# Optimization experiments

Hardware: AMD Instinct MI355X
Metric: run time of the kernel (lower is better)

The kernel has to match this reference:

```python
import jax, jax.numpy as jnp
import numpy as np

N = 50000     # num_nodes
E = 600000    # num_edges
H = 128       # h_dim
OUT = 32      # out_dim
R = 64        # num_rels
B = 16        # num_bases


def setup_inputs() -> dict:
    key = jax.random.key(0)
    ks = jax.random.split(key, 11)
    src = jax.random.randint(ks[0], (E,), 0, N)
    dst = jax.random.randint(ks[1], (E,), 0, N)
    etype = jax.random.randint(ks[2], (E,), 0, R)
    norm = jax.random.uniform(ks[3], (E, 1), dtype=jnp.float32)  # edge norm (e.g. 1/deg)
    emb = jax.random.normal(ks[4], (N, H), dtype=jnp.float32) * 0.05
    # basis-decomposed relation weights: W_r = sum_b comp[r,b] * V[b]
    V1 = jax.random.normal(ks[5], (B, H, H), dtype=jnp.float32) * (1.0 / np.sqrt(H))
    comp1 = jax.random.normal(ks[6], (R, B), dtype=jnp.float32) * (1.0 / np.sqrt(B))
    bias1 = jnp.zeros((H,), dtype=jnp.float32)
    V2 = jax.random.normal(ks[7], (B, H, OUT), dtype=jnp.float32) * (1.0 / np.sqrt(H))
    comp2 = jax.random.normal(ks[8], (R, B), dtype=jnp.float32) * (1.0 / np.sqrt(B))
    bias2 = jnp.zeros((OUT,), dtype=jnp.float32)
    return {"src": src, "dst": dst, "etype": etype, "norm": norm, "emb": emb,
            "V1": V1, "comp1": comp1, "bias1": bias1,
            "V2": V2, "comp2": comp2, "bias2": bias2}


def _rel_graph_conv(x, src, dst, etype, norm, V, comp, bias):
    # message for edge e: (x[src_e] @ W_{etype_e}) * norm_e, W_r = sum_b comp[r,b] V_b.
    # Since W is linear, fold norm into the gathered features, and aggregate
    # per (dst, basis) BEFORE the dense basis matmul (aggregate-first trick):
    #   agg[v, b] = sum_{e: dst_e=v} comp[etype_e, b] * norm_e * x[src_e]
    #   out[v]    = sum_b agg[v, b] @ V_b + bias
    xs = x[src] * norm                      # [E, in]
    w = comp[etype]                         # [E, B] per-edge basis coefficients
    # loop over the small fixed basis count (B=16), reusing the [E, in] buffer
    agg = jnp.stack(
        [jax.ops.segment_sum(xs * w[:, b:b + 1], dst, num_segments=N) for b in range(B)],
        axis=1,
    )                                       # [N, B, in]
    return jnp.einsum('nbi,bio->no', agg, V) + bias


def reference(src, dst, etype, norm, emb, V1, comp1, bias1, V2, comp2, bias2):
    h = _rel_graph_conv(emb, src, dst, etype, norm, V1, comp1, bias1)
    h = jax.nn.relu(h)                      # dropout p=0.0 -> identity
    h = _rel_graph_conv(h, src, dst, etype, norm, V2, comp2, bias2)
    return h
```

## Files before the change

kernel.cpp:

```cpp
#include <hip/hip_runtime.h>
#include <hip/hip_bf16.h>

#define NN 50000
#define EE 600000
#define HH 128
#define OUTD 32
#define RR 64
#define BB 16
#define KK 2048
#define SC_B ((NN + 1023) / 1024)
#define N_CONVW ((HH + OUTD) * KK)
#define N_EMB   (NN * HH / 2)

typedef short s16x8 __attribute__((ext_vector_type(8)));
typedef float f32x4 __attribute__((ext_vector_type(4)));
typedef float f32x2 __attribute__((ext_vector_type(2)));
typedef unsigned short ushort_t;
typedef unsigned int uint_t;
typedef __attribute__((address_space(3))) uint_t lds_u32;
typedef const __attribute__((address_space(1))) uint_t glb_u32;

__device__ inline ushort_t f_to_bf16(float f){
    __hip_bfloat16 h = __float2bfloat16(f);
    return *reinterpret_cast<ushort_t*>(&h);
}
__device__ inline uint_t pack_bf16x2(float a, float b){
    return (uint_t)f_to_bf16(a) | ((uint_t)f_to_bf16(b) << 16);
}

__global__ void hist_kernel(const int* __restrict__ dst, int* counts){
    int e = blockIdx.x*256 + threadIdx.x;
    if (e < EE) atomicAdd(&counts[dst[e]], 1);
}

__global__ void scan_part(const int* __restrict__ counts, int* __restrict__ tot){
    int b = blockIdx.x, t = threadIdx.x;
    int i0 = b*1024 + t*4;
    int s = 0;
    if (i0 + 3 < NN){
        int4 v = *reinterpret_cast<const int4*>(&counts[i0]);
        s = v.x + v.y + v.z + v.w;
    } else {
        for (int j = 0; j < 4; j++) if (i0 + j < NN) s += counts[i0 + j];
    }
    #pragma unroll
    for (int off = 32; off; off >>= 1) s += __shfl_xor(s, off, 64);
    __shared__ int ws[4];
    if ((t & 63) == 0) ws[t >> 6] = s;
    __syncthreads();
    if (t == 0) tot[b] = ws[0] + ws[1] + ws[2] + ws[3];
}

__global__ void scan_tot(int* tot){
    int t = threadIdx.x;
    int v = (t < SC_B) ? tot[t] : 0;
    int x = v;
    #pragma unroll
    for (int off = 1; off < 64; off <<= 1){
        int y = __shfl_up(x, off, 64);
        if (t >= off) x += y;
    }
    if (t < SC_B) tot[t] = x - v;
}

__global__ void scan_final(const int* __restrict__ counts, const int* __restrict__ tot,
                           int* __restrict__ offsets, int* __restrict__ cursor){
    int b = blockIdx.x, t = threadIdx.x, lane = t & 63, wv = t >> 6;
    int i0 = b*1024 + t*4;
    int v[4]; int s = 0;
    #pragma unroll
    for (int j = 0; j < 4; j++){ v[j] = (i0 + j < NN) ? counts[i0 + j] : 0; s += v[j]; }
    int x = s;
    #pragma unroll
    for (int off = 1; off < 64; off <<= 1){
        int y = __shfl_up(x, off, 64);
        if (lane >= off) x += y;
    }
    __shared__ int ws[4];
    if (lane == 63) ws[wv] = x;
    __syncthreads();
    int pre = tot[b];
    for (int i = 0; i < wv; i++) pre += ws[i];
    int run = pre + x - s;
    #pragma unroll
    for (int j = 0; j < 4; j++){
        if (i0 + j < NN){
            cursor[i0 + j] = run;
            offsets[i0 + j + 1] = run + v[j];
        }
        run += v[j];
    }
    if (b == 0 && t == 0) offsets[0] = 0;
}

__global__ void scatter_kernel(const int* __restrict__ dst, const int* __restrict__ src,
                               const int* __restrict__ etype, const float* __restrict__ norm,
                               int* cursor, int* __restrict__ msrc, int* __restrict__ netn){
    int e = blockIdx.x*256 + threadIdx.x;
    if (e >= EE) return;
    int d = dst[e];
    int r = atomicAdd(&cursor[d], 1);
    msrc[r] = src[e];
    netn[r] = (__float_as_int(norm[e]) & ~63) | etype[e];
}

__global__ void prep_kernel(const float* __restrict__ V1, const float* __restrict__ V2,
                            const float* __restrict__ emb,
                            ushort_t* __restrict__ Wt1, ushort_t* __restrict__ Wt2,
                            ushort_t* __restrict__ xb){
    int i = blockIdx.x*256 + threadIdx.x;
    if (i < HH*KK){
        int o = i / KK, k = i % KK;
        Wt1[i] = f_to_bf16(V1[(size_t)k*HH + o]);
    } else if (i < N_CONVW){
        int j = i - HH*KK;
        int o = j / KK, k = j % KK;
        Wt2[j] = f_to_bf16(V2[(size_t)k*OUTD + o]);
    } else if (i < N_CONVW + N_EMB){
        int j = i - N_CONVW;
        float2 f = *reinterpret_cast<const float2*>(emb + 2*(size_t)j);
        *reinterpret_cast<uint_t*>(xb + 2*(size_t)j) = pack_bf16x2(f.x, f.y);
    }
}

__global__ __launch_bounds__(256, 6) void agg_kernel(
    const ushort_t* __restrict__ xin, const int* __restrict__ msrc,
    const int* __restrict__ netn, const int* __restrict__ offsets,
    const float* __restrict__ comp, ushort_t* __restrict__ agg,
    int v0, int vc)
{
    int w = threadIdx.x >> 6, lane = threadIdx.x & 63;
    int v = v0 + blockIdx.x*4 + w;
    if (v >= v0 + vc) return;
    int p0 = offsets[v];
    int dd = offsets[v+1] - p0;
    const uint_t* xrow = reinterpret_cast<const uint_t*>(xin);

    f32x2 accA[8], accB[8];
    #pragma unroll
    for (int bp = 0; bp < 8; bp++){
        accA[bp].x = 0.f; accA[bp].y = 0.f;
        accB[bp].x = 0.f; accB[bp].y = 0.f;
    }

    for (int c0 = 0; c0 < dd; c0 += 64){
        int nc = min(64, dd - c0);
        int li = p0 + c0 + min(lane, nc - 1);
        int mp = msrc[li];
        int nr = netn[li];
        uint_t xr[8];
        #pragma unroll
        for (int j = 0; j < 8; ++j){
            int sr = __builtin_amdgcn_readlane(mp, min(j, nc - 1));
            xr[j] = xrow[(size_t)sr*64 + lane];
        }
        for (int eb = 0; eb < nc; eb += 8){
            #pragma unroll
            for (int j = 0; j < 8; ++j){
                int e = eb + j;
                int ec = min(e, nc - 1);
                int nb = __builtin_amdgcn_readlane(nr, ec);
                int et = nb & 63;
                float nw = (e < nc) ? __int_as_float(nb & ~63) : 0.f;
                uint_t u = xr[j];
                f32x2 xs;
                xs.x = __uint_as_float(u << 16) * nw;
                xs.y = __uint_as_float(u & 0xffff0000u) * nw;
                int en = e + 8;
                if (en < nc){
                    int srn = __builtin_amdgcn_readlane(mp, en);
                    xr[j] = xrow[(size_t)srn*64 + lane];
                }
                const f32x2* cp = reinterpret_cast<const f32x2*>(comp + et*BB);
                #pragma unroll
                for (int bp = 0; bp < 8; bp++){
                    f32x2 c2 = cp[bp];
                    asm("v_pk_fma_f32 %0, %1, %2, %0 op_sel:[0,0,0] op_sel_hi:[1,0,1]"
                        : "+v"(accA[bp]) : "s"(c2), "v"(xs));
                    asm("v_pk_fma_f32 %0, %1, %2, %0 op_sel:[0,1,0] op_sel_hi:[1,1,1]"
                        : "+v"(accB[bp]) : "s"(c2), "v"(xs));
                }
            }
        }
    }
    uint_t* arow = reinterpret_cast<uint_t*>(agg) + (size_t)(v - v0)*1024 + lane;
    #pragma unroll
    for (int b = 0; b < BB; b++){
        uint_t pk;
        asm("v_cvt_pk_bf16_f32 %0, %1, %2"
            : "=v"(pk) : "v"(accA[b>>1][b&1]), "v"(accB[b>>1][b&1]));
        arow[b*64] = pk;
    }
}

template<int BN, bool RELU, bool OUT_BF16>
__global__ __launch_bounds__(512, 6) void gemm_kernel(
    const ushort_t* __restrict__ A, const ushort_t* __restrict__ Wt,
    const float* __restrict__ bias, void* __restrict__ yout, int vc)
{
    __shared__ __align__(16) char Ald[2][64*128];
    __shared__ __align__(16) char Bld[2][BN*128];
    constexpr int CT = (BN == 128) ? 4 : 1;
    constexpr int NT = KK / 64;
    int tid = threadIdx.x, lane = tid & 63, lane15 = lane & 15;
    int w = tid >> 6;
    int wrbase = (BN == 128) ? (w >> 1)*16 : (w & 3)*16;
    int wcbase = (BN == 128) ? (w & 1)*64 : (w >> 2)*16;
    int m0 = blockIdx.x * 64;

    int rl = lane >> 3, jl = lane & 7;
    int ra = w*8 + rl;
    const ushort_t* agp = A + (size_t)(m0 + min(ra, vc-1))*KK + ((jl ^ (ra & 7))*8);
    const ushort_t* bgp0;
    const ushort_t* bgp1;
    if (BN == 128){
        int rb0 = w*16 + rl, rb1 = w*16 + 8 + rl;
        bgp0 = Wt + (size_t)rb0*KK + ((jl ^ (rb0 & 7))*8);
        bgp1 = Wt + (size_t)rb1*KK + ((jl ^ (rb1 & 7))*8);
    } else {
        int rb = w*8 + rl;
        bgp0 = Wt + (size_t)min(rb, BN-1)*KK + ((jl ^ (rb & 7))*8);
        bgp1 = nullptr;
    }

    auto stage = [&](int buf){
        __builtin_amdgcn_global_load_lds((glb_u32*)agp,
            (lds_u32*)(&Ald[buf][w*1024]), 16, 0, 0);
        agp += 64;
        if constexpr (BN == 128){
            __builtin_amdgcn_global_load_lds((glb_u32*)bgp0,
                (lds_u32*)(&Bld[buf][w*2048]), 16, 0, 0);
            __builtin_amdgcn_global_load_lds((glb_u32*)bgp1,
                (lds_u32*)(&Bld[buf][w*2048 + 1024]), 16, 0, 0);
            bgp0 += 64; bgp1 += 64;
        } else {
            if (w < 4){
                __builtin_amdgcn_global_load_lds((glb_u32*)bgp0,
                    (lds_u32*)(&Bld[buf][w*1024]), 16, 0, 0);
                bgp0 += 64;
            }
        }
    };

    f32x4 acc[CT];
    #pragma unroll
    for (int ct = 0; ct < CT; ct++)
        #pragma unroll
        for (int j = 0; j < 4; j++) acc[ct][j] = 0.f;

    auto compute = [&](int buf){
        #pragma unroll
        for (int ks = 0; ks < 2; ks++){
            int csw = (ks*4 + (lane >> 4)) ^ (lane15 & 7);
            int arow = wrbase + lane15;
            s16x8 a = *reinterpret_cast<const s16x8*>(&Ald[buf][arow*128 + csw*16]);
            #pragma unroll
            for (int ct = 0; ct < CT; ct++){
                int brow = wcbase + ct*16 + lane15;
                s16x8 b = *reinterpret_cast<const s16x8*>(&Bld[buf][brow*128 + csw*16]);
                acc[ct] = __builtin_amdgcn_mfma_f32_16x16x32_bf16(a, b, acc[ct], 0,0,0);
            }
        }
    };

    stage(0);
    for (int t = 0; t < NT; ++t){
        int cur = t & 1;
        if (t + 1 < NT){
            stage(cur ^ 1);
            if (BN == 128)       asm volatile("s_waitcnt vmcnt(3)" ::: "memory");
            else if (w < 4)      asm volatile("s_waitcnt vmcnt(2)" ::: "memory");
            else                 asm volatile("s_waitcnt vmcnt(1)" ::: "memory");
        } else {
            asm volatile("s_waitcnt vmcnt(0)" ::: "memory");
        }
        __builtin_amdgcn_s_barrier();
        __builtin_amdgcn_sched_barrier(0);
        compute(cur);
        __builtin_amdgcn_s_barrier();
    }

    int rb = m0 + wrbase + ((lane >> 4) << 2);
    #pragma unroll
    for (int ct = 0; ct < CT; ct++){
        int col = wcbase + ct*16 + lane15;
        float bv = bias[col];
        #pragma unroll
        for (int r = 0; r < 4; r++){
            int row = rb + r;
            if (row < vc){
                float val = acc[ct][r] + bv;
                if (RELU) val = fmaxf(val, 0.f);
                if (OUT_BF16)
                    reinterpret_cast<ushort_t*>(yout)[(size_t)row*BN + col] = f_to_bf16(val);
                else
                    reinterpret_cast<float*>(yout)[(size_t)row*BN + col] = val;
            }
        }
    }
}

extern "C" void kernel_launch(void* const* d_in, const int* in_sizes, int n_in,
                              void* d_out, int out_size, void* d_ws, size_t ws_size,
                              hipStream_t stream){
    const int*   src   = (const int*)d_in[0];
    const int*   dst   = (const int*)d_in[1];
    const int*   etype = (const int*)d_in[2];
    const float* norm  = (const float*)d_in[3];
    const float* emb   = (const float*)d_in[4];
    const float* V1    = (const float*)d_in[5];
    const float* comp1 = (const float*)d_in[6];
    const float* bias1 = (const float*)d_in[7];
    const float* V2    = (const float*)d_in[8];
    const float* comp2 = (const float*)d_in[9];
    const float* bias2 = (const float*)d_in[10];
    float* out = (float*)d_out;

    char* w = (char*)d_ws;
    auto alloc = [&](size_t bytes) -> char* {
        char* p = w; w += (bytes + 255) & ~(size_t)255; return p;
    };
    int*      offsets = (int*)alloc((NN + 1) * 4);
    int*      counts  = (int*)alloc(NN * 4);
    int*      cursor  = (int*)alloc(NN * 4);
    int*      tot     = (int*)alloc(SC_B * 4);
    int*      msrc    = (int*)alloc((size_t)EE * 4);
    int*      netn    = (int*)alloc((size_t)EE * 4);
    ushort_t* Wt1     = (ushort_t*)alloc((size_t)HH * KK * 2);
    ushort_t* Wt2     = (ushort_t*)alloc((size_t)OUTD * KK * 2);
    ushort_t* xb      = (ushort_t*)alloc((size_t)NN * HH * 2);
    ushort_t* h       = (ushort_t*)alloc((size_t)NN * HH * 2);
    size_t used  = (size_t)(w - (char*)d_ws);
    size_t avail = ws_size > used ? ws_size - used : 0;
    int chunkN = (int)(avail / ((size_t)KK * 2));
    chunkN &= ~127;
    if (chunkN < 128) chunkN = 128;
    if (chunkN > NN) chunkN = NN;
    ushort_t* agg = (ushort_t*)w;

    hipMemsetAsync(counts, 0, NN * 4, stream);
    hist_kernel<<<(EE + 255)/256, 256, 0, stream>>>(dst, counts);
    scan_part<<<SC_B, 256, 0, stream>>>(counts, tot);
    scan_tot<<<1, 64, 0, stream>>>(tot);
    scan_final<<<SC_B, 256, 0, stream>>>(counts, tot, offsets, cursor);
    scatter_kernel<<<(EE + 255)/256, 256, 0, stream>>>(dst, src, etype, norm,
                                                       cursor, msrc, netn);
    prep_kernel<<<(N_CONVW + N_EMB + 255)/256, 256, 0, stream>>>(
        V1, V2, emb, Wt1, Wt2, xb);

    for (int v0 = 0; v0 < NN; v0 += chunkN){
        int vc = (NN - v0 < chunkN) ? (NN - v0) : chunkN;
        agg_kernel<<<(vc + 3)/4, 256, 0, stream>>>(
            xb, msrc, netn, offsets, comp1, agg, v0, vc);
        gemm_kernel<HH, true, true><<<(vc + 63)/64, 512, 0, stream>>>(
            agg, Wt1, bias1, h + (size_t)v0 * HH, vc);
    }
    for (int v0 = 0; v0 < NN; v0 += chunkN){
        int vc = (NN - v0 < chunkN) ? (NN - v0) : chunkN;
        agg_kernel<<<(vc + 3)/4, 256, 0, stream>>>(
            h, msrc, netn, offsets, comp2, agg, v0, vc);
        gemm_kernel<OUTD, false, false><<<(vc + 63)/64, 512, 0, stream>>>(
            agg, Wt2, bias2, out + (size_t)v0 * OUTD, vc);
    }
}
```

Before: 302.5 us.

## Store aggregation and weight matrices in pre-tiled swizzled layout for contiguous GEMM staging

```diff
diff --git a/kernel.cpp b/kernel.cpp
--- a/kernel.cpp
+++ b/kernel.cpp
@@ -11,6 +11,7 @@
 #define SC_B ((NN + 1023) / 1024)
 #define N_CONVW ((HH + OUTD) * KK)
 #define N_EMB   (NN * HH / 2)
+#define TILEB   262144
 
 typedef short s16x8 __attribute__((ext_vector_type(8)));
 typedef float f32x4 __attribute__((ext_vector_type(4)));
@@ -111,11 +112,17 @@
     int i = blockIdx.x*256 + threadIdx.x;
     if (i < HH*KK){
         int o = i / KK, k = i % KK;
-        Wt1[i] = f_to_bf16(V1[(size_t)k*HH + o]);
+        size_t addr = (size_t)(k >> 6)*16384 + (size_t)o*128
+                    + ((((k & 63) >> 3) ^ (o & 7)) << 4) + (k & 7)*2;
+        *reinterpret_cast<ushort_t*>(reinterpret_cast<char*>(Wt1) + addr) =
+            f_to_bf16(V1[(size_t)k*HH + o]);
     } else if (i < N_CONVW){
         int j = i - HH*KK;
         int o = j / KK, k = j % KK;
-        Wt2[j] = f_to_bf16(V2[(size_t)k*OUTD + o]);
+        size_t addr = (size_t)(k >> 6)*4096 + (size_t)o*128
+                    + ((((k & 63) >> 3) ^ (o & 7)) << 4) + (k & 7)*2;
+        *reinterpret_cast<ushort_t*>(reinterpret_cast<char*>(Wt2) + addr) =
+            f_to_bf16(V2[(size_t)k*OUTD + o]);
     } else if (i < N_CONVW + N_EMB){
         int j = i - N_CONVW;
         float2 f = *reinterpret_cast<const float2*>(emb + 2*(size_t)j);
@@ -183,13 +190,19 @@
             }
         }
     }
-    uint_t* arow = reinterpret_cast<uint_t*>(agg) + (size_t)(v - v0)*1024 + lane;
-    #pragma unroll
-    for (int b = 0; b < BB; b++){
-        uint_t pk;
-        asm("v_cvt_pk_bf16_f32 %0, %1, %2"
-            : "=v"(pk) : "v"(accA[b>>1][b&1]), "v"(accB[b>>1][b&1]));
-        arow[b*64] = pk;
+    {
+        int idx = v - v0;
+        int r = idx & 63;
+        char* tbase = reinterpret_cast<char*>(agg) + (size_t)(idx >> 6)*TILEB + r*128;
+        int goff = ((((lane & 31) >> 2) ^ (r & 7)) << 4) + (lane & 3)*4;
+        #pragma unroll
+        for (int b = 0; b < BB; b++){
+            uint_t pk;
+            asm("v_cvt_pk_bf16_f32 %0, %1, %2"
+                : "=v"(pk) : "v"(accA[b>>1][b&1]), "v"(accB[b>>1][b&1]));
+            int kc = b*2 + (lane >> 5);
+            *reinterpret_cast<uint_t*>(tbase + kc*8192 + goff) = pk;
+        }
     }
 }
 
@@ -202,42 +215,34 @@
     __shared__ __align__(16) char Bld[2][BN*128];
     constexpr int CT = (BN == 128) ? 4 : 1;
     constexpr int NT = KK / 64;
+    constexpr int BSTRIDE = BN * 128;
     int tid = threadIdx.x, lane = tid & 63, lane15 = lane & 15;
     int w = tid >> 6;
     int wrbase = (BN == 128) ? (w >> 1)*16 : (w & 3)*16;
     int wcbase = (BN == 128) ? (w & 1)*64 : (w >> 2)*16;
     int m0 = blockIdx.x * 64;
 
-    int rl = lane >> 3, jl = lane & 7;
-    int ra = w*8 + rl;
-    const ushort_t* agp = A + (size_t)(m0 + min(ra, vc-1))*KK + ((jl ^ (ra & 7))*8);
-    const ushort_t* bgp0;
-    const ushort_t* bgp1;
-    if (BN == 128){
-        int rb0 = w*16 + rl, rb1 = w*16 + 8 + rl;
-        bgp0 = Wt + (size_t)rb0*KK + ((jl ^ (rb0 & 7))*8);
-        bgp1 = Wt + (size_t)rb1*KK + ((jl ^ (rb1 & 7))*8);
-    } else {
-        int rb = w*8 + rl;
-        bgp0 = Wt + (size_t)min(rb, BN-1)*KK + ((jl ^ (rb & 7))*8);
-        bgp1 = nullptr;
-    }
+    const char* agp = reinterpret_cast<const char*>(A) + (size_t)blockIdx.x*TILEB
+                    + w*1024 + lane*16;
+    const char* bgp0 = reinterpret_cast<const char*>(Wt)
+                     + ((BN == 128) ? (w*2048) : (w*1024)) + lane*16;
+    const char* bgp1 = reinterpret_cast<const char*>(Wt) + w*2048 + 1024 + lane*16;
 
     auto stage = [&](int buf){
         __builtin_amdgcn_global_load_lds((glb_u32*)agp,
             (lds_u32*)(&Ald[buf][w*1024]), 16, 0, 0);
-        agp += 64;
+        agp += 8192;
         if constexpr (BN == 128){
             __builtin_amdgcn_global_load_lds((glb_u32*)bgp0,
                 (lds_u32*)(&Bld[buf][w*2048]), 16, 0, 0);
             __builtin_amdgcn_global_load_lds((glb_u32*)bgp1,
                 (lds_u32*)(&Bld[buf][w*2048 + 1024]), 16, 0, 0);
-            bgp0 += 64; bgp1 += 64;
+            bgp0 += BSTRIDE; bgp1 += BSTRIDE;
         } else {
             if (w < 4){
                 __builtin_amdgcn_global_load_lds((glb_u32*)bgp0,
                     (lds_u32*)(&Bld[buf][w*1024]), 16, 0, 0);
-                bgp0 += 64;
+                bgp0 += BSTRIDE;
             }
         }
     };
```

Result: no change. 304.6 us (+0.7%).
